# Optimization experiments

Hardware: AMD Instinct MI355X
Metric: run time of the kernel (lower is better)

The kernel has to match this reference:

```python
import jax, jax.numpy as jnp
import numpy as np

U, I, D = 100000, 150000, 64
N = U + I
E = 1250000
KEEP_RATE = 0.8


def setup_inputs() -> dict:
    key = jax.random.key(0)
    k1, k2, k3, k4, k5, k6 = jax.random.split(key, 6)
    row = jax.random.randint(k1, (E,), 0, N, dtype=jnp.int32)
    col = jax.random.randint(k2, (E,), 0, N, dtype=jnp.int32)
    adj_values = jax.random.uniform(k3, (E,), dtype=jnp.float32)
    # edge dropout mask: floor(rand + keep_rate) in {0,1}, exactly as SpAdjEdgeDrop
    edge_mask = jnp.floor(jax.random.uniform(k4, (E,), dtype=jnp.float32) + KEEP_RATE)
    user_embeds = jax.random.normal(k5, (U, D), dtype=jnp.float32)
    item_embeds = jax.random.normal(k6, (I, D), dtype=jnp.float32)
    return {
        "row": row,
        "col": col,
        "adj_values": adj_values,
        "edge_mask": edge_mask,
        "user_embeds": user_embeds,
        "item_embeds": item_embeds,
        "layer_num": 3,
    }


def reference(row, col, adj_values, edge_mask, user_embeds, item_embeds, layer_num):
    user_num = user_embeds.shape[0]
    n_nodes = user_num + item_embeds.shape[0]
    # edge-dropped sparse values (mask==0 edges contribute nothing to spmm)
    vals = adj_values * edge_mask  # [E]
    embeds = jnp.concatenate([user_embeds, item_embeds], axis=0)  # [N, D]
    acc = embeds
    cur = embeds
    for _ in range(layer_num):
        # spmm: out[r] += vals[e] * cur[c] for each edge e=(r,c)
        msgs = vals[:, None] * cur[col]  # [E, D] gather
        cur = jax.ops.segment_sum(msgs, row, num_segments=n_nodes)  # [N, D] scatter-add
        acc = acc + cur
    out = acc / (layer_num + 1)
    return out[:user_num], out[user_num:]
```

## Files before the change

### kernel.cpp

```cpp
#include <hip/hip_runtime.h>


#define U_NODES 100000
#define N_NODES 250000
#define DIM4 16
#define E_EDGES 1250000
#define SCAN_TILE 1024

typedef unsigned short u16;

__device__ __forceinline__ float bf2f(u16 h) {
    return __uint_as_float(((unsigned)h) << 16);
}
__device__ __forceinline__ u16 f2bf(float f) {
    unsigned u = __float_as_uint(f);
    u += 0x7fffu + ((u >> 16) & 1u);
    return (u16)(u >> 16);
}
__device__ __forceinline__ ushort4 gat(const u16* __restrict__ base, int node, int part) {
    return ((const ushort4*)(base + ((size_t)node << 6)))[part];
}
__device__ __forceinline__ void fma4(float4& s, float v, ushort4 h) {
    s.x += v * bf2f(h.x);
    s.y += v * bf2f(h.y);
    s.z += v * bf2f(h.z);
    s.w += v * bf2f(h.w);
}

__global__ void lgcn_convert(const float4* __restrict__ user4,
                             const float4* __restrict__ item4,
                             u16* __restrict__ e0b) {
    long i = (long)blockIdx.x * blockDim.x + threadIdx.x;
    const long total = (long)N_NODES * DIM4;
    if (i >= total) return;
    const long uc = (long)U_NODES * DIM4;
    float4 v = (i < uc) ? user4[i] : item4[i - uc];
    ((ushort4*)e0b)[i] = make_ushort4(f2bf(v.x), f2bf(v.y), f2bf(v.z), f2bf(v.w));
}

__global__ void lgcn_count(const int* __restrict__ row,
                           const float* __restrict__ mask,
                           int* __restrict__ counts,
                           int* __restrict__ epos) {
    int e = blockIdx.x * blockDim.x + threadIdx.x;
    if (e >= E_EDGES) return;
    if (mask[e] != 0.0f) epos[e] = atomicAdd(&counts[row[e]], 1);
}

__global__ void lgcn_offsets(const int* __restrict__ counts,
                             int2* __restrict__ rowdesc,
                             int* __restrict__ total) {
    __shared__ int lds[256];
    __shared__ int sbase;
    int t = threadIdx.x;
    int base = blockIdx.x * SCAN_TILE + t * 4;
    int4 c = make_int4(0, 0, 0, 0);
    if (base + 3 < N_NODES) {
        c = *(const int4*)(counts + base);
    } else {
        if (base + 0 < N_NODES) c.x = counts[base + 0];
        if (base + 1 < N_NODES) c.y = counts[base + 1];
        if (base + 2 < N_NODES) c.z = counts[base + 2];
        if (base + 3 < N_NODES) c.w = counts[base + 3];
    }
    int4 p = make_int4((c.x + 3) & ~3, (c.y + 3) & ~3, (c.z + 3) & ~3, (c.w + 3) & ~3);
    int s = p.x + p.y + p.z + p.w;
    lds[t] = s;
    __syncthreads();
    for (int off = 1; off < 256; off <<= 1) {
        int v = (t >= off) ? lds[t - off] : 0;
        __syncthreads();
        if (t >= off) lds[t] += v;
        __syncthreads();
    }
    if (t == 255) sbase = atomicAdd(total, lds[255]);
    __syncthreads();
    int pos = sbase + lds[t] - s;
    if (base + 0 < N_NODES) rowdesc[base + 0] = make_int2(pos, c.x); pos += p.x;
    if (base + 1 < N_NODES) rowdesc[base + 1] = make_int2(pos, c.y); pos += p.y;
    if (base + 2 < N_NODES) rowdesc[base + 2] = make_int2(pos, c.z); pos += p.z;
    if (base + 3 < N_NODES) rowdesc[base + 3] = make_int2(pos, c.w);
}

__global__ void lgcn_fill(const int* __restrict__ row,
                          const int* __restrict__ col,
                          const float* __restrict__ adj,
                          const float* __restrict__ mask,
                          const int2* __restrict__ rowdesc,
                          const int* __restrict__ epos,
                          int2* __restrict__ csr) {
    int e = blockIdx.x * blockDim.x + threadIdx.x;
    if (e >= E_EDGES) return;
    float m = mask[e];
    if (m == 0.0f) return;
    int2 rd = rowdesc[row[e]];
    int rank = epos[e];
    csr[rd.x + rank] = make_int2(col[e], __float_as_int(adj[e] * m));
    if (rank == rd.y - 1) {
        int pe = (rd.y + 3) & ~3;
        for (int p = rd.y; p < pe; ++p) csr[rd.x + p] = make_int2(0, 0);
    }
}

template <bool LAST>
__global__ void lgcn_pull(const int2* __restrict__ rowdesc,
                          const int2* __restrict__ csr,
                          const u16*  __restrict__ curb,
                          const u16*  __restrict__ e0b,
                          const u16*  __restrict__ e1b,
                          u16*        __restrict__ outb,
                          float4*     __restrict__ out) {
    int tid = blockIdx.x * blockDim.x + threadIdx.x;
    int r = tid >> 4;
    int part = tid & 15;
    if (r >= N_NODES) return;
    int2 rd = rowdesc[r];
    int start = rd.x;
    int pend  = start + ((rd.y + 3) & ~3);
    float4 s = make_float4(0.f, 0.f, 0.f, 0.f);
    int e = start;
    for (; e + 8 <= pend; e += 8) {
        int4 ca = *(const int4*)(csr + e);
        int4 cb = *(const int4*)(csr + e + 2);
        int4 cc = *(const int4*)(csr + e + 4);
        int4 cd = *(const int4*)(csr + e + 6);
        ushort4 h0 = gat(curb, ca.x, part);
        ushort4 h1 = gat(curb, ca.z, part);
        ushort4 h2 = gat(curb, cb.x, part);
        ushort4 h3 = gat(curb, cb.z, part);
        ushort4 h4 = gat(curb, cc.x, part);
        ushort4 h5 = gat(curb, cc.z, part);
        ushort4 h6 = gat(curb, cd.x, part);
        ushort4 h7 = gat(curb, cd.z, part);
        fma4(s, __int_as_float(ca.y), h0);
        fma4(s, __int_as_float(ca.w), h1);
        fma4(s, __int_as_float(cb.y), h2);
        fma4(s, __int_as_float(cb.w), h3);
        fma4(s, __int_as_float(cc.y), h4);
        fma4(s, __int_as_float(cc.w), h5);
        fma4(s, __int_as_float(cd.y), h6);
        fma4(s, __int_as_float(cd.w), h7);
    }
    if (e < pend) {
        int4 ca = *(const int4*)(csr + e);
        int4 cb = *(const int4*)(csr + e + 2);
        ushort4 h0 = gat(curb, ca.x, part);
        ushort4 h1 = gat(curb, ca.z, part);
        ushort4 h2 = gat(curb, cb.x, part);
        ushort4 h3 = gat(curb, cb.z, part);
        fma4(s, __int_as_float(ca.y), h0);
        fma4(s, __int_as_float(ca.w), h1);
        fma4(s, __int_as_float(cb.y), h2);
        fma4(s, __int_as_float(cb.w), h3);
    }
    size_t oi = (size_t)r * DIM4 + part;
    if (LAST) {
        ushort4 a0 = ((const ushort4*)e0b)[oi];
        ushort4 a1 = ((const ushort4*)e1b)[oi];
        ushort4 a2 = ((const ushort4*)curb)[oi];
        out[oi] = make_float4(
            (s.x + bf2f(a0.x) + bf2f(a1.x) + bf2f(a2.x)) * 0.25f,
            (s.y + bf2f(a0.y) + bf2f(a1.y) + bf2f(a2.y)) * 0.25f,
            (s.z + bf2f(a0.z) + bf2f(a1.z) + bf2f(a2.z)) * 0.25f,
            (s.w + bf2f(a0.w) + bf2f(a1.w) + bf2f(a2.w)) * 0.25f);
    } else {
        ((ushort4*)outb)[oi] = make_ushort4(f2bf(s.x), f2bf(s.y), f2bf(s.z), f2bf(s.w));
    }
}

extern "C" void kernel_launch(void* const* d_in, const int* in_sizes, int n_in,
                              void* d_out, int out_size, void* d_ws, size_t ws_size,
                              hipStream_t stream) {
    const int*   row  = (const int*)d_in[0];
    const int*   col  = (const int*)d_in[1];
    const float* adj  = (const float*)d_in[2];
    const float* mask = (const float*)d_in[3];
    const float4* user4 = (const float4*)d_in[4];
    const float4* item4 = (const float4*)d_in[5];

    float4* acc = (float4*)d_out;

    const size_t bemb_bytes = (size_t)N_NODES * 64 * sizeof(u16);
    char* p = (char*)d_ws;
    u16* e0b = (u16*)p;  p += bemb_bytes;
    u16* e1b = (u16*)p;  p += bemb_bytes;
    u16* e2b = (u16*)p;  p += bemb_bytes;
    int* total   = (int*)p;
    int* counts  = (int*)(p + 64);
    p += 64 + (((size_t)N_NODES * 4) + 63) & ~63ul;
    int2* rowdesc = (int2*)p;  p += (((size_t)N_NODES * 8) + 63) & ~63ul;
    int*  epos    = (int*)p;   p += (((size_t)E_EDGES * 4) + 63) & ~63ul;
    int2* csr     = (int2*)p;

    const int BLK = 256;
    const long node_vec4 = (long)N_NODES * DIM4;
    const int  grid_node = (int)((node_vec4 + BLK - 1) / BLK);
    const int  grid_edge = (E_EDGES + BLK - 1) / BLK;
    const int  nblk_scan = (N_NODES + SCAN_TILE - 1) / SCAN_TILE;

    hipMemsetAsync(total, 0, 64 + (size_t)N_NODES * sizeof(int), stream);
    lgcn_convert<<<grid_node, BLK, 0, stream>>>(user4, item4, e0b);
    lgcn_count<<<grid_edge, BLK, 0, stream>>>(row, mask, counts, epos);
    lgcn_offsets<<<nblk_scan, BLK, 0, stream>>>(counts, rowdesc, total);
    lgcn_fill<<<grid_edge, BLK, 0, stream>>>(row, col, adj, mask, rowdesc, epos, csr);

    lgcn_pull<false><<<grid_node, BLK, 0, stream>>>(rowdesc, csr, e0b, nullptr, nullptr, e1b, nullptr);
    lgcn_pull<false><<<grid_node, BLK, 0, stream>>>(rowdesc, csr, e1b, nullptr, nullptr, e2b, nullptr);
    lgcn_pull<true ><<<grid_node, BLK, 0, stream>>>(rowdesc, csr, e2b, e0b, e1b, nullptr, acc);
}
```

Measured before the change: 328.5 us.

## Sort rows by degree bucket and gather 16-byte chunks with 8 threads per row

Adds a degree-bucketing pass: the offsets kernel counts rows per padded-degree bucket, and a new permutation kernel writes row descriptors sorted by descending degree. The pull kernels then walk this permuted order, so rows of similar length share a wavefront and less time is lost to divergence. Each row is now handled by 8 threads, each loading 16-byte bf16 chunks instead of 8-byte ones, which halves the threads per row and widens each memory access. The cost is an extra kernel, more workspace, and output writes that are scattered because rows come out of order.

```diff
diff --git a/kernel.cpp b/kernel.cpp
--- a/kernel.cpp
+++ b/kernel.cpp
@@ -6,25 +6,33 @@
 #define DIM4 16
 #define E_EDGES 1250000
 #define SCAN_TILE 1024
+#define NBUCKET 32
 
 typedef unsigned short u16;
 
-__device__ __forceinline__ float bf2f(u16 h) {
-    return __uint_as_float(((unsigned)h) << 16);
-}
 __device__ __forceinline__ u16 f2bf(float f) {
     unsigned u = __float_as_uint(f);
     u += 0x7fffu + ((u >> 16) & 1u);
     return (u16)(u >> 16);
 }
-__device__ __forceinline__ ushort4 gat(const u16* __restrict__ base, int node, int part) {
-    return ((const ushort4*)(base + ((size_t)node << 6)))[part];
-}
-__device__ __forceinline__ void fma4(float4& s, float v, ushort4 h) {
-    s.x += v * bf2f(h.x);
-    s.y += v * bf2f(h.y);
-    s.z += v * bf2f(h.z);
-    s.w += v * bf2f(h.w);
+__device__ __forceinline__ float blo(unsigned u) {
+    return __uint_as_float(u << 16);
+}
+__device__ __forceinline__ float bhi(unsigned u) {
+    return __uint_as_float(u & 0xffff0000u);
+}
+__device__ __forceinline__ int4 gat16(const u16* __restrict__ base, int node, int part) {
+    return ((const int4*)(base + ((size_t)node << 6)))[part];
+}
+__device__ __forceinline__ void fma8(float4& sa, float4& sb, float v, int4 h) {
+    sa.x += v * blo((unsigned)h.x);
+    sa.y += v * bhi((unsigned)h.x);
+    sa.z += v * blo((unsigned)h.y);
+    sa.w += v * bhi((unsigned)h.y);
+    sb.x += v * blo((unsigned)h.z);
+    sb.y += v * bhi((unsigned)h.z);
+    sb.z += v * blo((unsigned)h.w);
+    sb.w += v * bhi((unsigned)h.w);
 }
 
 __global__ void lgcn_convert(const float4* __restrict__ user4,
@@ -49,10 +57,16 @@
 
 __global__ void lgcn_offsets(const int* __restrict__ counts,
                              int2* __restrict__ rowdesc,
-                             int* __restrict__ total) {
+                             int* __restrict__ total,
+                             int* __restrict__ bcount,
+                             int* __restrict__ rowpos) {
     __shared__ int lds[256];
     __shared__ int sbase;
+    __shared__ int lbc[NBUCKET];
+    __shared__ int lbb[NBUCKET];
     int t = threadIdx.x;
+    if (t < NBUCKET) lbc[t] = 0;
+    __syncthreads();
     int base = blockIdx.x * SCAN_TILE + t * 4;
     int4 c = make_int4(0, 0, 0, 0);
     if (base + 3 < N_NODES) {
@@ -65,8 +79,18 @@
     }
     int4 p = make_int4((c.x + 3) & ~3, (c.y + 3) & ~3, (c.z + 3) & ~3, (c.w + 3) & ~3);
     int s = p.x + p.y + p.z + p.w;
+    int b0 = (c.x + 3) >> 2; if (b0 > NBUCKET - 1) b0 = NBUCKET - 1;
+    int b1 = (c.y + 3) >> 2; if (b1 > NBUCKET - 1) b1 = NBUCKET - 1;
+    int b2 = (c.z + 3) >> 2; if (b2 > NBUCKET - 1) b2 = NBUCKET - 1;
+    int b3 = (c.w + 3) >> 2; if (b3 > NBUCKET - 1) b3 = NBUCKET - 1;
+    int l0 = 0, l1 = 0, l2 = 0, l3 = 0;
+    if (base + 0 < N_NODES) l0 = atomicAdd(&lbc[b0], 1);
+    if (base + 1 < N_NODES) l1 = atomicAdd(&lbc[b1], 1);
+    if (base + 2 < N_NODES) l2 = atomicAdd(&lbc[b2], 1);
+    if (base + 3 < N_NODES) l3 = atomicAdd(&lbc[b3], 1);
     lds[t] = s;
     __syncthreads();
+    if (t < NBUCKET) lbb[t] = atomicAdd(&bcount[t], lbc[t]);
     for (int off = 1; off < 256; off <<= 1) {
         int v = (t >= off) ? lds[t - off] : 0;
         __syncthreads();
@@ -76,10 +100,28 @@
     if (t == 255) sbase = atomicAdd(total, lds[255]);
     __syncthreads();
     int pos = sbase + lds[t] - s;
-    if (base + 0 < N_NODES) rowdesc[base + 0] = make_int2(pos, c.x); pos += p.x;
-    if (base + 1 < N_NODES) rowdesc[base + 1] = make_int2(pos, c.y); pos += p.y;
-    if (base + 2 < N_NODES) rowdesc[base + 2] = make_int2(pos, c.z); pos += p.z;
-    if (base + 3 < N_NODES) rowdesc[base + 3] = make_int2(pos, c.w);
+    if (base + 0 < N_NODES) { rowdesc[base + 0] = make_int2(pos, c.x); rowpos[base + 0] = ((lbb[b0] + l0) << 5) | b0; } pos += p.x;
+    if (base + 1 < N_NODES) { rowdesc[base + 1] = make_int2(pos, c.y); rowpos[base + 1] = ((lbb[b1] + l1) << 5) | b1; } pos += p.y;
+    if (base + 2 < N_NODES) { rowdesc[base + 2] = make_int2(pos, c.z); rowpos[base + 2] = ((lbb[b2] + l2) << 5) | b2; } pos += p.z;
+    if (base + 3 < N_NODES) { rowdesc[base + 3] = make_int2(pos, c.w); rowpos[base + 3] = ((lbb[b3] + l3) << 5) | b3; }
+}
+
+__global__ void lgcn_perm(const int* __restrict__ bcount,
+                          const int* __restrict__ rowpos,
+                          const int2* __restrict__ rowdesc,
+                          int4* __restrict__ permdesc) {
+    __shared__ int bb[NBUCKET];
+    int t = threadIdx.x;
+    if (t == 0) {
+        int s = 0;
+        for (int i = NBUCKET - 1; i >= 0; --i) { bb[i] = s; s += bcount[i]; }
+    }
+    __syncthreads();
+    int r = blockIdx.x * blockDim.x + t;
+    if (r >= N_NODES) return;
+    int pk = rowpos[r];
+    int2 rd = rowdesc[r];
+    permdesc[bb[pk & 31] + (pk >> 5)] = make_int4(rd.x, rd.y, r, 0);
 }
 
 __global__ void lgcn_fill(const int* __restrict__ row,
@@ -103,7 +145,7 @@
 }
 
 template <bool LAST>
-__global__ void lgcn_pull(const int2* __restrict__ rowdesc,
+__global__ void lgcn_pull(const int4* __restrict__ permdesc,
                           const int2* __restrict__ csr,
                           const u16*  __restrict__ curb,
                           const u16*  __restrict__ e0b,
@@ -111,60 +153,72 @@
                           u16*        __restrict__ outb,
                           float4*     __restrict__ out) {
     int tid = blockIdx.x * blockDim.x + threadIdx.x;
-    int r = tid >> 4;
-    int part = tid & 15;
-    if (r >= N_NODES) return;
-    int2 rd = rowdesc[r];
-    int start = rd.x;
-    int pend  = start + ((rd.y + 3) & ~3);
-    float4 s = make_float4(0.f, 0.f, 0.f, 0.f);
+    int g = tid >> 3;
+    if (g >= N_NODES) return;
+    int part = tid & 7;
+    int4 d = permdesc[g];
+    int start = d.x;
+    int pend  = start + ((d.y + 3) & ~3);
+    float4 sa = make_float4(0.f, 0.f, 0.f, 0.f);
+    float4 sb = make_float4(0.f, 0.f, 0.f, 0.f);
     int e = start;
     for (; e + 8 <= pend; e += 8) {
         int4 ca = *(const int4*)(csr + e);
         int4 cb = *(const int4*)(csr + e + 2);
         int4 cc = *(const int4*)(csr + e + 4);
         int4 cd = *(const int4*)(csr + e + 6);
-        ushort4 h0 = gat(curb, ca.x, part);
-        ushort4 h1 = gat(curb, ca.z, part);
-        ushort4 h2 = gat(curb, cb.x, part);
-        ushort4 h3 = gat(curb, cb.z, part);
-        ushort4 h4 = gat(curb, cc.x, part);
-        ushort4 h5 = gat(curb, cc.z, part);
-        ushort4 h6 = gat(curb, cd.x, part);
-        ushort4 h7 = gat(curb, cd.z, part);
-        fma4(s, __int_as_float(ca.y), h0);
-        fma4(s, __int_as_float(ca.w), h1);
-        fma4(s, __int_as_float(cb.y), h2);
-        fma4(s, __int_as_float(cb.w), h3);
-        fma4(s, __int_as_float(cc.y), h4);
-        fma4(s, __int_as_float(cc.w), h5);
-        fma4(s, __int_as_float(cd.y), h6);
-        fma4(s, __int_as_float(cd.w), h7);
+        int4 h0 = gat16(curb, ca.x, part);
+        int4 h1 = gat16(curb, ca.z, part);
+        int4 h2 = gat16(curb, cb.x, part);
+        int4 h3 = gat16(curb, cb.z, part);
+        int4 h4 = gat16(curb, cc.x, part);
+        int4 h5 = gat16(curb, cc.z, part);
+        int4 h6 = gat16(curb, cd.x, part);
+        int4 h7 = gat16(curb, cd.z, part);
+        fma8(sa, sb, __int_as_float(ca.y), h0);
+        fma8(sa, sb, __int_as_float(ca.w), h1);
+        fma8(sa, sb, __int_as_float(cb.y), h2);
+        fma8(sa, sb, __int_as_float(cb.w), h3);
+        fma8(sa, sb, __int_as_float(cc.y), h4);
+        fma8(sa, sb, __int_as_float(cc.w), h5);
+        fma8(sa, sb, __int_as_float(cd.y), h6);
+        fma8(sa, sb, __int_as_float(cd.w), h7);
     }
     if (e < pend) {
         int4 ca = *(const int4*)(csr + e);
         int4 cb = *(const int4*)(csr + e + 2);
-        ushort4 h0 = gat(curb, ca.x, part);
-        ushort4 h1 = gat(curb, ca.z, part);
-        ushort4 h2 = gat(curb, cb.x, part);
-        ushort4 h3 = gat(curb, cb.z, part);
-        fma4(s, __int_as_float(ca.y), h0);
-        fma4(s, __int_as_float(ca.w), h1);
-        fma4(s, __int_as_float(cb.y), h2);
-        fma4(s, __int_as_float(cb.w), h3);
-    }
-    size_t oi = (size_t)r * DIM4 + part;
+        int4 h0 = gat16(curb, ca.x, part);
+        int4 h1 = gat16(curb, ca.z, part);
+        int4 h2 = gat16(curb, cb.x, part);
+        int4 h3 = gat16(curb, cb.z, part);
+        fma8(sa, sb, __int_as_float(ca.y), h0);
+        fma8(sa, sb, __int_as_float(ca.w), h1);
+        fma8(sa, sb, __int_as_float(cb.y), h2);
+        fma8(sa, sb, __int_as_float(cb.w), h3);
+    }
+    int r = d.z;
+    size_t oi = (size_t)r * 8 + part;
     if (LAST) {
-        ushort4 a0 = ((const ushort4*)e0b)[oi];
-        ushort4 a1 = ((const ushort4*)e1b)[oi];
-        ushort4 a2 = ((const ushort4*)curb)[oi];
-        out[oi] = make_float4(
-            (s.x + bf2f(a0.x) + bf2f(a1.x) + bf2f(a2.x)) * 0.25f,
-            (s.y + bf2f(a0.y) + bf2f(a1.y) + bf2f(a2.y)) * 0.25f,
-            (s.z + bf2f(a0.z) + bf2f(a1.z) + bf2f(a2.z)) * 0.25f,
-            (s.w + bf2f(a0.w) + bf2f(a1.w) + bf2f(a2.w)) * 0.25f);
+        int4 a0 = ((const int4*)e0b)[oi];
+        int4 a1 = ((const int4*)e1b)[oi];
+        int4 a2 = ((const int4*)curb)[oi];
+        float4 o0, o1;
+        o0.x = (sa.x + blo((unsigned)a0.x) + blo((unsigned)a1.x) + blo((unsigned)a2.x)) * 0.25f;
+        o0.y = (sa.y + bhi((unsigned)a0.x) + bhi((unsigned)a1.x) + bhi((unsigned)a2.x)) * 0.25f;
+        o0.z = (sa.z + blo((unsigned)a0.y) + blo((unsigned)a1.y) + blo((unsigned)a2.y)) * 0.25f;
+        o0.w = (sa.w + bhi((unsigned)a0.y) + bhi((unsigned)a1.y) + bhi((unsigned)a2.y)) * 0.25f;
+        o1.x = (sb.x + blo((unsigned)a0.z) + blo((unsigned)a1.z) + blo((unsigned)a2.z)) * 0.25f;
+        o1.y = (sb.y + bhi((unsigned)a0.z) + bhi((unsigned)a1.z) + bhi((unsigned)a2.z)) * 0.25f;
+        o1.z = (sb.z + blo((unsigned)a0.w) + blo((unsigned)a1.w) + blo((unsigned)a2.w)) * 0.25f;
+        o1.w = (sb.w + bhi((unsigned)a0.w) + bhi((unsigned)a1.w) + bhi((unsigned)a2.w)) * 0.25f;
+        out[(size_t)r * 16 + part * 2]     = o0;
+        out[(size_t)r * 16 + part * 2 + 1] = o1;
     } else {
-        ((ushort4*)outb)[oi] = make_ushort4(f2bf(s.x), f2bf(s.y), f2bf(s.z), f2bf(s.w));
+        unsigned p0 = (unsigned)f2bf(sa.x) | ((unsigned)f2bf(sa.y) << 16);
+        unsigned p1 = (unsigned)f2bf(sa.z) | ((unsigned)f2bf(sa.w) << 16);
+        unsigned p2 = (unsigned)f2bf(sb.x) | ((unsigned)f2bf(sb.y) << 16);
+        unsigned p3 = (unsigned)f2bf(sb.z) | ((unsigned)f2bf(sb.w) << 16);
+        ((int4*)outb)[oi] = make_int4((int)p0, (int)p1, (int)p2, (int)p3);
     }
 }
 
@@ -185,26 +239,33 @@
     u16* e0b = (u16*)p;  p += bemb_bytes;
     u16* e1b = (u16*)p;  p += bemb_bytes;
     u16* e2b = (u16*)p;  p += bemb_bytes;
-    int* total   = (int*)p;
-    int* counts  = (int*)(p + 64);
-    p += 64 + (((size_t)N_NODES * 4) + 63) & ~63ul;
-    int2* rowdesc = (int2*)p;  p += (((size_t)N_NODES * 8) + 63) & ~63ul;
-    int*  epos    = (int*)p;   p += (((size_t)E_EDGES * 4) + 63) & ~63ul;
-    int2* csr     = (int2*)p;
+    int* total  = (int*)p;
+    int* bcount = (int*)(p + 64);
+    int* counts = (int*)(p + 256);
+    p += 256 + (((size_t)N_NODES * 4 + 63) & ~63ul);
+    int2* rowdesc  = (int2*)p;  p += ((size_t)N_NODES * 8 + 63) & ~63ul;
+    int*  rowpos   = (int*)p;   p += ((size_t)N_NODES * 4 + 63) & ~63ul;
+    int*  epos     = (int*)p;   p += ((size_t)E_EDGES * 4 + 63) & ~63ul;
+    int4* permdesc = (int4*)p;  p += ((size_t)N_NODES * 16 + 63) & ~63ul;
+    int2* csr      = (int2*)p;
 
     const int BLK = 256;
     const long node_vec4 = (long)N_NODES * DIM4;
-    const int  grid_node = (int)((node_vec4 + BLK - 1) / BLK);
+    const int  grid_conv = (int)((node_vec4 + BLK - 1) / BLK);
     const int  grid_edge = (E_EDGES + BLK - 1) / BLK;
     const int  nblk_scan = (N_NODES + SCAN_TILE - 1) / SCAN_TILE;
-
-    hipMemsetAsync(total, 0, 64 + (size_t)N_NODES * sizeof(int), stream);
-    lgcn_convert<<<grid_node, BLK, 0, stream>>>(user4, item4, e0b);
+    const int  grid_perm = (N_NODES + BLK - 1) / BLK;
+    const long pull_thr  = (long)N_NODES * 8;
+    const int  grid_pull = (int)((pull_thr + BLK - 1) / BLK);
+
+    hipMemsetAsync(total, 0, 256 + (size_t)N_NODES * sizeof(int), stream);
+    lgcn_convert<<<grid_conv, BLK, 0, stream>>>(user4, item4, e0b);
     lgcn_count<<<grid_edge, BLK, 0, stream>>>(row, mask, counts, epos);
-    lgcn_offsets<<<nblk_scan, BLK, 0, stream>>>(counts, rowdesc, total);
+    lgcn_offsets<<<nblk_scan, BLK, 0, stream>>>(counts, rowdesc, total, bcount, rowpos);
+    lgcn_perm<<<grid_perm, BLK, 0, stream>>>(bcount, rowpos, rowdesc, permdesc);
     lgcn_fill<<<grid_edge, BLK, 0, stream>>>(row, col, adj, mask, rowdesc, epos, csr);
 
-    lgcn_pull<false><<<grid_node, BLK, 0, stream>>>(rowdesc, csr, e0b, nullptr, nullptr, e1b, nullptr);
-    lgcn_pull<false><<<grid_node, BLK, 0, stream>>>(rowdesc, csr, e1b, nullptr, nullptr, e2b, nullptr);
-    lgcn_pull<true ><<<grid_node, BLK, 0, stream>>>(rowdesc, csr, e2b, e0b, e1b, nullptr, acc);
-}
+    lgcn_pull<false><<<grid_pull, BLK, 0, stream>>>(permdesc, csr, e0b, nullptr, nullptr, e1b, nullptr);
+    lgcn_pull<false><<<grid_pull, BLK, 0, stream>>>(permdesc, csr, e1b, nullptr, nullptr, e2b, nullptr);
+    lgcn_pull<true ><<<grid_pull, BLK, 0, stream>>>(permdesc, csr, e2b, e0b, e1b, nullptr, acc);
+}
```

New measurement: 326.3 us. Within noise of the previous version (-0.7%).
